# Optimization experiments

Hardware: AMD Instinct MI355X
Metric: run time of the kernel (lower is better)

Reference implementation:

```python
import jax, jax.numpy as jnp
import numpy as np

D_MODEL = 1536
BLOCK = 3
N_BLOCKS = D_MODEL // BLOCK
BATCH = 8192
EPS = 1e-8


def setup_inputs() -> dict:
    key = jax.random.key(0)
    ks = jax.random.split(key, 6)
    s = 1.0 / np.sqrt(D_MODEL)  # torch Linear default-ish scale
    x = jax.random.normal(ks[0], (BATCH, D_MODEL), dtype=jnp.float32)
    h_prev = jax.random.normal(ks[1], (BATCH, D_MODEL), dtype=jnp.float32)
    W_biv = jax.random.normal(ks[2], (D_MODEL, D_MODEL), dtype=jnp.float32) * s
    b_biv = jnp.zeros((D_MODEL,), dtype=jnp.float32)  # init.zeros_
    W_dec = jax.random.normal(ks[3], (1, D_MODEL), dtype=jnp.float32) * s
    b_dec = jnp.full((1,), 1.4, dtype=jnp.float32)  # init.constant_(1.4)
    W_in = jax.random.normal(ks[4], (D_MODEL, D_MODEL), dtype=jnp.float32) * s
    b_in = jax.random.normal(ks[5], (D_MODEL,), dtype=jnp.float32) * s
    return {"x": x, "h_prev": h_prev, "W_biv": W_biv, "b_biv": b_biv,
            "W_dec": W_dec, "b_dec": b_dec, "W_in": W_in, "b_in": b_in}


def _quat_rotate_blocks(h_blocks, bivectors):
    # h_blocks, bivectors: (batch, n_blocks, 3)
    norm_b = jnp.maximum(jnp.linalg.norm(bivectors, axis=-1, keepdims=True), EPS)
    half_angle = norm_b / 2
    w = jnp.cos(half_angle)[..., 0]
    s = (jnp.sin(half_angle) / norm_b)[..., 0]  # sin_ha_over_norm[..., 0]
    # NOTE: faithful to source — qx/qy/qz all use component 0 of sin_ha_over_norm
    qx = s * bivectors[..., 2]
    qy = -s * bivectors[..., 1]
    qz = s * bivectors[..., 0]
    vx, vy, vz = h_blocks[..., 0], h_blocks[..., 1], h_blocks[..., 2]
    tx = 2 * (qy * vz - qz * vy)
    ty = 2 * (qz * vx - qx * vz)
    tz = 2 * (qx * vy - qy * vx)
    rx = vx + w * tx + (qy * tz - qz * ty)
    ry = vy + w * ty + (qz * tx - qx * tz)
    rz = vz + w * tz + (qx * ty - qy * tx)
    return jnp.stack([rx, ry, rz], axis=-1)


def reference(x, h_prev, W_biv, b_biv, W_dec, b_dec, W_in, b_in):
    batch = x.shape[0]
    bivectors = (x @ W_biv.T + b_biv).reshape(batch, N_BLOCKS, 3)
    decay = jax.nn.sigmoid(x @ W_dec.T + b_dec)          # (batch, 1)
    injection = x @ W_in.T + b_in                        # (batch, d_model)
    h_blocks = h_prev.reshape(batch, N_BLOCKS, 3)
    rotated = _quat_rotate_blocks(h_blocks, bivectors)
    return decay * rotated.reshape(batch, D_MODEL) + injection
```

## Files before the change

### kernel.cpp

```cpp
#include <hip/hip_runtime.h>
#include <cstdint>

#define D_MODEL 1536
#define BATCH   8192
#define EPS     1e-8f

#define BM 128
#define BN 96
#define BK 64
#define NT (D_MODEL / BK)
#define NTN (D_MODEL / BN)
#define NTM (BATCH / BM)
#define BUF 40960

typedef __attribute__((ext_vector_type(8))) short bf16x8;
typedef __attribute__((ext_vector_type(8))) unsigned short ushort8;
typedef __attribute__((ext_vector_type(4))) float f32x4;

__device__ __forceinline__ unsigned short f2bf(float f) {
  unsigned u = __builtin_bit_cast(unsigned, f);
  u += 0x7fffu + ((u >> 16) & 1u);
  return (unsigned short)(u >> 16);
}

__device__ __forceinline__ ushort8 pack8u(float4 a, float4 b) {
  ushort8 o;
  o[0] = f2bf(a.x); o[1] = f2bf(a.y); o[2] = f2bf(a.z); o[3] = f2bf(a.w);
  o[4] = f2bf(b.x); o[5] = f2bf(b.y); o[6] = f2bf(b.z); o[7] = f2bf(b.w);
  return o;
}

__device__ __forceinline__ void full_drain() {
  asm volatile("s_waitcnt vmcnt(0) lgkmcnt(0)" ::: "memory");
}
__device__ __forceinline__ void vm_drain() {
  asm volatile("s_waitcnt vmcnt(0)" ::: "memory");
}
__device__ __forceinline__ void lgkm_drain() {
  asm volatile("s_waitcnt lgkmcnt(0)" ::: "memory");
}

__device__ __forceinline__ void load_lds16(const void* g, void* l) {
  __builtin_amdgcn_global_load_lds(
      (const __attribute__((address_space(1))) unsigned int*)g,
      (__attribute__((address_space(3))) unsigned int*)l,
      16, 0, 0);
}

__global__ void prep_all(const float* __restrict__ x,
                         const float* __restrict__ wdec,
                         const float* __restrict__ bdec,
                         const float* __restrict__ wbiv,
                         const float* __restrict__ win,
                         unsigned short* __restrict__ xb,
                         unsigned short* __restrict__ wb,
                         float* __restrict__ decay) {
  const int b = blockIdx.x;
  if (b < 2048) {
    int row  = (int)((b * 256 + threadIdx.x) >> 6);
    int lane = threadIdx.x & 63;
    const float4* xr = (const float4*)(x + (long)row * D_MODEL);
    const float4* wr = (const float4*)wdec;
    unsigned short* xo = xb + (long)row * D_MODEL;
    float acc = 0.f;
#pragma unroll
    for (int i = 0; i < 6; ++i) {
      float4 a = xr[lane + 64 * i];
      float4 w = wr[lane + 64 * i];
      acc += a.x * w.x + a.y * w.y + a.z * w.z + a.w * w.w;
      ushort4 o;
      o.x = f2bf(a.x); o.y = f2bf(a.y); o.z = f2bf(a.z); o.w = f2bf(a.w);
      *(ushort4*)(xo + (lane + 64 * i) * 4) = o;
    }
    for (int off = 32; off; off >>= 1) acc += __shfl_xor(acc, off);
    if (lane == 0) decay[row] = 1.f / (1.f + expf(-(acc + bdec[0])));
  } else {
    const long NW4 = (long)D_MODEL * D_MODEL / 4;
    for (long i = (long)(b - 2048) * 256 + threadIdx.x; i < 2 * NW4;
         i += (long)1024 * 256) {
      const float4* src = (i < NW4) ? (const float4*)wbiv : (const float4*)win;
      long j = (i < NW4) ? i : (i - NW4);
      float4 v = src[j];
      ushort4 o;
      o.x = f2bf(v.x); o.y = f2bf(v.y); o.z = f2bf(v.z); o.w = f2bf(v.w);
      *(ushort4*)(wb + 4 * i) = o;
    }
  }
}

__global__ __launch_bounds__(512, 2)
void fused_main(const unsigned short* __restrict__ xb,
                const unsigned short* __restrict__ wb,
                const float* __restrict__ hprev,
                const float* __restrict__ decay,
                const float* __restrict__ bbiv,
                const float* __restrict__ bin,
                float* __restrict__ out) {
  __shared__ __align__(16) char smem[2 * BUF];
  float* sBv = (float*)smem;

  const int bid = blockIdx.x;
  const int tm = bid / NTN, tn = bid % NTN;
  const int m0 = tm * BM, n0 = tn * BN;
  const int tid  = threadIdx.x;
  const int lane = tid & 63, wid = tid >> 6;
  const int wr = wid >> 1, wc = wid & 1;
  const int lr = lane & 15;
  const int lk = lane >> 4;

  const unsigned short* gptr[5];
  int doff[5];
#pragma unroll
  for (int i = 0; i < 5; ++i) {
    int f = i * 512 + tid;
    if (f < 1024) {
      int row = f >> 3, c = f & 7, cs = c ^ (row & 7);
      gptr[i] = xb + (long)(m0 + row) * D_MODEL + cs * 8;
      doff[i] = f << 4;
    } else if (f < 1792) {
      int g = f - 1024;
      int row = g >> 3, c = g & 7, cs = c ^ (row & 7);
      gptr[i] = wb + (long)(n0 + row) * D_MODEL + cs * 8;
      doff[i] = 16384 + (g << 4);
    } else {
      int g = f - 1792;
      int row = g >> 3, c = g & 7, cs = c ^ (row & 7);
      gptr[i] = wb + (long)D_MODEL * D_MODEL + (long)(n0 + row) * D_MODEL + cs * 8;
      doff[i] = 28672 + (g << 4);
    }
  }

  auto STAGE = [&](int bb) {
#pragma unroll
    for (int i = 0; i < 5; ++i) {
      load_lds16(gptr[i], smem + bb + doff[i]);
      gptr[i] += BK;
    }
  };

  int offA[2][2], offB1[3][2], offB2[3][2];
#pragma unroll
  for (int ks = 0; ks < 2; ++ks) {
    const int slot = ks * 4 + lk;
#pragma unroll
    for (int mi = 0; mi < 2; ++mi) {
      int R = wr * 32 + mi * 16 + lr;
      offA[mi][ks] = (R * 64 + (slot ^ (R & 7)) * 8) * 2;
    }
#pragma unroll
    for (int ni = 0; ni < 3; ++ni) {
      int R = wc * 48 + ni * 16 + lr;
      int o = (R * 64 + (slot ^ (R & 7)) * 8) * 2;
      offB1[ni][ks] = 16384 + o;
      offB2[ni][ks] = 28672 + o;
    }
  }

  f32x4 accB[2][3], accI[2][3];
#pragma unroll
  for (int a = 0; a < 2; ++a)
#pragma unroll
    for (int b = 0; b < 3; ++b) { accB[a][b] = (f32x4)0.f; accI[a][b] = (f32x4)0.f; }

  STAGE(0);
  vm_drain();
  __syncthreads();

  for (int t = 0; t < NT; ++t) {
    const int cur = (t & 1) * BUF;
    if (t + 1 < NT) STAGE(((t + 1) & 1) * BUF);

#pragma unroll
    for (int ks = 0; ks < 2; ++ks) {
      bf16x8 a[2], b1[3], b2[3];
#pragma unroll
      for (int mi = 0; mi < 2; ++mi)
        a[mi] = *(const bf16x8*)(smem + cur + offA[mi][ks]);
#pragma unroll
      for (int ni = 0; ni < 3; ++ni) {
        b1[ni] = *(const bf16x8*)(smem + cur + offB1[ni][ks]);
        b2[ni] = *(const bf16x8*)(smem + cur + offB2[ni][ks]);
      }
      lgkm_drain();
      __builtin_amdgcn_sched_barrier(0);
#pragma unroll
      for (int mi = 0; mi < 2; ++mi)
#pragma unroll
        for (int ni = 0; ni < 3; ++ni)
          accB[mi][ni] = __builtin_amdgcn_mfma_f32_16x16x32_bf16(
              a[mi], b1[ni], accB[mi][ni], 0, 0, 0);
      __builtin_amdgcn_sched_barrier(0);
#pragma unroll
      for (int mi = 0; mi < 2; ++mi)
#pragma unroll
        for (int ni = 0; ni < 3; ++ni)
          accI[mi][ni] = __builtin_amdgcn_mfma_f32_16x16x32_bf16(
              a[mi], b2[ni], accI[mi][ni], 0, 0, 0);
      __builtin_amdgcn_sched_barrier(0);
    }

    vm_drain();
    __syncthreads();
  }

#pragma unroll
  for (int mi = 0; mi < 2; ++mi)
#pragma unroll
    for (int ni = 0; ni < 3; ++ni) {
      int col = wc * 48 + ni * 16 + lr;
      float bb = bbiv[n0 + col];
#pragma unroll
      for (int r = 0; r < 4; ++r) {
        int row = wr * 32 + mi * 16 + lk * 4 + r;
        sBv[row * 97 + col] = accB[mi][ni][r] + bb;
      }
    }
  full_drain();
  __syncthreads();

#pragma unroll
  for (int mi = 0; mi < 2; ++mi)
#pragma unroll
    for (int ni = 0; ni < 3; ++ni) {
      int col  = wc * 48 + ni * 16 + lr;
      int gcol = n0 + col;
      int c    = (col % 3);
      int lc0  = col - c;
      float binv = bin[gcol];
#pragma unroll
      for (int r = 0; r < 4; ++r) {
        int row  = wr * 32 + mi * 16 + lk * 4 + r;
        int grow = m0 + row;
        float bx = sBv[row * 97 + lc0];
        float by = sBv[row * 97 + lc0 + 1];
        float bz = sBv[row * 97 + lc0 + 2];
        const float* hp = hprev + (long)grow * D_MODEL + (n0 + lc0);
        float vx = hp[0], vy = hp[1], vz = hp[2];
        float nb = sqrtf(bx * bx + by * by + bz * bz);
        nb = fmaxf(nb, EPS);
        float ha = 0.5f * nb;
        float w  = __cosf(ha);
        float s  = __sinf(ha) / nb;
        float qx = s * bz, qy = -s * by, qz = s * bx;
        float tx = 2.f * (qy * vz - qz * vy);
        float ty = 2.f * (qz * vx - qx * vz);
        float tz = 2.f * (qx * vy - qy * vx);
        float rx = vx + w * tx + (qy * tz - qz * ty);
        float ry = vy + w * ty + (qz * tx - qx * tz);
        float rz = vz + w * tz + (qx * ty - qy * tx);
        float rc = (c == 0) ? rx : ((c == 1) ? ry : rz);
        out[(long)grow * D_MODEL + gcol] =
            decay[grow] * rc + (accI[mi][ni][r] + binv);
      }
    }
}

__global__ __launch_bounds__(256, 2)
void fused_mfma3(const float* __restrict__ x,
                 const float* __restrict__ wbiv,
                 const float* __restrict__ win,
                 const float* __restrict__ hprev,
                 const float* __restrict__ wdec,
                 const float* __restrict__ bdec,
                 const float* __restrict__ bbiv,
                 const float* __restrict__ bin,
                 float* __restrict__ out) {
  __shared__ __align__(16) char smem[50688];
  __shared__ float sDecay[BM];
  unsigned short* sA  = (unsigned short*)smem;
  unsigned short* sB1 = (unsigned short*)(smem + 16384);
  unsigned short* sB2 = (unsigned short*)(smem + 28672);
  float* sBv = (float*)smem;

  const int bid = blockIdx.x;
  const int tm = bid / NTN, tn = bid % NTN;
  const int m0 = tm * BM, n0 = tn * BN;
  const int tid  = threadIdx.x;
  const int lane = tid & 63, wid = tid >> 6;
  const int wr = wid >> 1, wc = wid & 1;
  const int lr = lane & 15;
  const int lk = lane >> 4;

  {
    const float bd = bdec[0];
    const float4* wd4 = (const float4*)wdec;
    for (int rr = 0; rr < 32; ++rr) {
      int row = wid * 32 + rr;
      const float4* xr = (const float4*)(x + (long)(m0 + row) * D_MODEL);
      float acc = 0.f;
#pragma unroll
      for (int i = 0; i < 6; ++i) {
        float4 a = xr[lane + 64 * i];
        float4 b = wd4[lane + 64 * i];
        acc += a.x * b.x + a.y * b.y + a.z * b.z + a.w * b.w;
      }
      for (int off = 32; off; off >>= 1) acc += __shfl_xor(acc, off);
      if (lane == 0) sDecay[row] = 1.f / (1.f + expf(-(acc + bd)));
    }
  }

  f32x4 accB[4][3], accI[4][3];
#pragma unroll
  for (int a = 0; a < 4; ++a)
#pragma unroll
    for (int b = 0; b < 3; ++b) { accB[a][b] = (f32x4)0.f; accI[a][b] = (f32x4)0.f; }

  for (int kt = 0; kt < D_MODEL; kt += 64) {
    full_drain();
    __syncthreads();
#pragma unroll
    for (int i = 0; i < 4; ++i) {
      int f = i * 256 + tid;
      int row = f >> 3, c = f & 7;
      const float4* p = (const float4*)(x + (long)(m0 + row) * D_MODEL + kt + c * 8);
      *(ushort8*)(sA + row * 64 + c * 8) = pack8u(p[0], p[1]);
    }
#pragma unroll
    for (int i = 0; i < 6; ++i) {
      int mat = (i >= 3);
      int g = (i - 3 * mat) * 256 + tid;
      int row = g >> 3, c = g & 7;
      const float* wsrc = mat ? win : wbiv;
      const float4* p = (const float4*)(wsrc + (long)(n0 + row) * D_MODEL + kt + c * 8);
      *(ushort8*)((mat ? sB2 : sB1) + row * 64 + c * 8) = pack8u(p[0], p[1]);
    }
    full_drain();
    __syncthreads();

#pragma unroll
    for (int ks = 0; ks < 2; ++ks) {
      const int k0 = ks * 32 + lk * 8;
      bf16x8 a[4], b1[3], b2[3];
#pragma unroll
      for (int mi = 0; mi < 4; ++mi)
        a[mi] = *(const bf16x8*)(sA + (wr * 64 + mi * 16 + lr) * 64 + k0);
#pragma unroll
      for (int ni = 0; ni < 3; ++ni) {
        b1[ni] = *(const bf16x8*)(sB1 + (wc * 48 + ni * 16 + lr) * 64 + k0);
        b2[ni] = *(const bf16x8*)(sB2 + (wc * 48 + ni * 16 + lr) * 64 + k0);
      }
      full_drain();
      __builtin_amdgcn_sched_barrier(0);
#pragma unroll
      for (int mi = 0; mi < 4; ++mi)
#pragma unroll
        for (int ni = 0; ni < 3; ++ni)
          accB[mi][ni] = __builtin_amdgcn_mfma_f32_16x16x32_bf16(
              a[mi], b1[ni], accB[mi][ni], 0, 0, 0);
      __builtin_amdgcn_sched_barrier(0);
#pragma unroll
      for (int mi = 0; mi < 4; ++mi)
#pragma unroll
        for (int ni = 0; ni < 3; ++ni)
          accI[mi][ni] = __builtin_amdgcn_mfma_f32_16x16x32_bf16(
              a[mi], b2[ni], accI[mi][ni], 0, 0, 0);
      __builtin_amdgcn_sched_barrier(0);
    }
  }

  full_drain();
  __syncthreads();
#pragma unroll
  for (int mi = 0; mi < 4; ++mi)
#pragma unroll
    for (int ni = 0; ni < 3; ++ni) {
      int col = wc * 48 + ni * 16 + lr;
      float bb = bbiv[n0 + col];
#pragma unroll
      for (int r = 0; r < 4; ++r) {
        int row = wr * 64 + mi * 16 + lk * 4 + r;
        sBv[row * 97 + col] = accB[mi][ni][r] + bb;
      }
    }
  full_drain();
  __syncthreads();

#pragma unroll
  for (int mi = 0; mi < 4; ++mi)
#pragma unroll
    for (int ni = 0; ni < 3; ++ni) {
      int col  = wc * 48 + ni * 16 + lr;
      int gcol = n0 + col;
      int c    = (col % 3);
      int lc0  = col - c;
      float binv = bin[gcol];
#pragma unroll
      for (int r = 0; r < 4; ++r) {
        int row  = wr * 64 + mi * 16 + lk * 4 + r;
        int grow = m0 + row;
        float bx = sBv[row * 97 + lc0];
        float by = sBv[row * 97 + lc0 + 1];
        float bz = sBv[row * 97 + lc0 + 2];
        const float* hp = hprev + (long)grow * D_MODEL + (n0 + lc0);
        float vx = hp[0], vy = hp[1], vz = hp[2];
        float nb = sqrtf(bx * bx + by * by + bz * bz);
        nb = fmaxf(nb, EPS);
        float ha = 0.5f * nb;
        float w  = cosf(ha);
        float s  = sinf(ha) / nb;
        float qx = s * bz, qy = -s * by, qz = s * bx;
        float tx = 2.f * (qy * vz - qz * vy);
        float ty = 2.f * (qz * vx - qx * vz);
        float tz = 2.f * (qx * vy - qy * vx);
        float rx = vx + w * tx + (qy * tz - qz * ty);
        float ry = vy + w * ty + (qz * tx - qx * tz);
        float rz = vz + w * tz + (qx * ty - qy * tx);
        float rc = (c == 0) ? rx : ((c == 1) ? ry : rz);
        out[(long)grow * D_MODEL + gcol] =
            sDecay[row] * rc + (accI[mi][ni][r] + binv);
      }
    }
}

extern "C" void kernel_launch(void* const* d_in, const int* in_sizes, int n_in,
                              void* d_out, int out_size, void* d_ws, size_t ws_size,
                              hipStream_t stream) {
  const float* x     = (const float*)d_in[0];
  const float* hprev = (const float*)d_in[1];
  const float* wbiv  = (const float*)d_in[2];
  const float* bbiv  = (const float*)d_in[3];
  const float* wdec  = (const float*)d_in[4];
  const float* bdec  = (const float*)d_in[5];
  const float* win   = (const float*)d_in[6];
  const float* bin   = (const float*)d_in[7];
  float* out = (float*)d_out;

  const size_t XB_B  = 25165824;
  const size_t WB_B  = 9437184;
  const size_t DC_B  = 32768;

  if (ws_size >= XB_B + WB_B + DC_B) {
    char* ws = (char*)d_ws;
    unsigned short* xb = (unsigned short*)ws;
    unsigned short* wb = (unsigned short*)(ws + XB_B);
    float* decay       = (float*)(ws + XB_B + WB_B);
    prep_all<<<dim3(3072), dim3(256), 0, stream>>>(
        x, wdec, bdec, wbiv, win, xb, wb, decay);
    fused_main<<<dim3(NTM * NTN), dim3(512), 0, stream>>>(
        xb, wb, hprev, decay, bbiv, bin, out);
  } else {
    fused_mfma3<<<dim3(NTM * NTN), dim3(256), 0, stream>>>(
        x, wbiv, win, hprev, wdec, bdec, bbiv, bin, out);
  }
}
```

Measured before the change: 113.5 us.

## Double M tile to 256 rows with 1024-thread blocks for weight reuse

Raises the fused GEMM block tile from 128 to 256 batch rows and uses 16 waves per block, so each staged tile of the two weight matrices is shared by twice as many rows. The aim is to cut global and LDS traffic for weights per output element. In exchange, occupancy drops to one block per CU, the LDS footprint grows to about 112 KB, and the grid halves, which may worsen latency hiding and tail balance.

Measured after the change: 113.2 us (median of 2 runs). No clear change (-0.3%).

```diff
diff --git a/kernel.cpp b/kernel.cpp
--- a/kernel.cpp
+++ b/kernel.cpp
@@ -5,13 +5,15 @@
 #define BATCH   8192
 #define EPS     1e-8f
 
+#define BMM 256
+#define BN  96
+#define BK  64
+#define NT  (D_MODEL / BK)
+#define NTN (D_MODEL / BN)
+#define NTMM (BATCH / BMM)
+#define BUF 57344
 #define BM 128
-#define BN 96
-#define BK 64
-#define NT (D_MODEL / BK)
-#define NTN (D_MODEL / BN)
 #define NTM (BATCH / BM)
-#define BUF 40960
 
 typedef __attribute__((ext_vector_type(8))) short bf16x8;
 typedef __attribute__((ext_vector_type(8))) unsigned short ushort8;
@@ -88,7 +90,7 @@
   }
 }
 
-__global__ __launch_bounds__(512, 2)
+__global__ __launch_bounds__(1024, 1)
 void fused_main(const unsigned short* __restrict__ xb,
                 const unsigned short* __restrict__ wb,
                 const float* __restrict__ hprev,
@@ -96,46 +98,53 @@
                 const float* __restrict__ bbiv,
                 const float* __restrict__ bin,
                 float* __restrict__ out) {
-  __shared__ __align__(16) char smem[2 * BUF];
+  __shared__ __align__(16) char smem[114688];
   float* sBv = (float*)smem;
 
   const int bid = blockIdx.x;
   const int tm = bid / NTN, tn = bid % NTN;
-  const int m0 = tm * BM, n0 = tn * BN;
+  const int m0 = tm * BMM, n0 = tn * BN;
   const int tid  = threadIdx.x;
   const int lane = tid & 63, wid = tid >> 6;
   const int wr = wid >> 1, wc = wid & 1;
   const int lr = lane & 15;
   const int lk = lane >> 4;
 
-  const unsigned short* gptr[5];
-  int doff[5];
-#pragma unroll
-  for (int i = 0; i < 5; ++i) {
-    int f = i * 512 + tid;
-    if (f < 1024) {
+  const unsigned short* gptr[4];
+  int doff[4];
+  {
+#pragma unroll
+    for (int i = 0; i < 2; ++i) {
+      int f = i * 1024 + tid;
       int row = f >> 3, c = f & 7, cs = c ^ (row & 7);
       gptr[i] = xb + (long)(m0 + row) * D_MODEL + cs * 8;
       doff[i] = f << 4;
-    } else if (f < 1792) {
-      int g = f - 1024;
+    }
+    if (tid < 768) {
+      int g = tid;
       int row = g >> 3, c = g & 7, cs = c ^ (row & 7);
-      gptr[i] = wb + (long)(n0 + row) * D_MODEL + cs * 8;
-      doff[i] = 16384 + (g << 4);
+      gptr[2] = wb + (long)(n0 + row) * D_MODEL + cs * 8;
+      doff[2] = 32768 + (g << 4);
     } else {
-      int g = f - 1792;
+      int g = tid - 768;
       int row = g >> 3, c = g & 7, cs = c ^ (row & 7);
-      gptr[i] = wb + (long)D_MODEL * D_MODEL + (long)(n0 + row) * D_MODEL + cs * 8;
-      doff[i] = 28672 + (g << 4);
+      gptr[2] = wb + (long)D_MODEL * D_MODEL + (long)(n0 + row) * D_MODEL + cs * 8;
+      doff[2] = 45056 + (g << 4);
+    }
+    {
+      int g = 256 + tid;
+      int row = g >> 3, c = g & 7, cs = c ^ (row & 7);
+      gptr[3] = wb + (long)D_MODEL * D_MODEL + (long)(n0 + row) * D_MODEL + cs * 8;
+      doff[3] = 45056 + (g << 4);
     }
   }
 
   auto STAGE = [&](int bb) {
-#pragma unroll
-    for (int i = 0; i < 5; ++i) {
-      load_lds16(gptr[i], smem + bb + doff[i]);
-      gptr[i] += BK;
-    }
+    load_lds16(gptr[0], smem + bb + doff[0]);
+    load_lds16(gptr[1], smem + bb + doff[1]);
+    load_lds16(gptr[2], smem + bb + doff[2]);
+    if (tid < 512) load_lds16(gptr[3], smem + bb + doff[3]);
+    gptr[0] += BK; gptr[1] += BK; gptr[2] += BK; gptr[3] += BK;
   };
 
   int offA[2][2], offB1[3][2], offB2[3][2];
@@ -151,8 +160,8 @@
     for (int ni = 0; ni < 3; ++ni) {
       int R = wc * 48 + ni * 16 + lr;
       int o = (R * 64 + (slot ^ (R & 7)) * 8) * 2;
-      offB1[ni][ks] = 16384 + o;
-      offB2[ni][ks] = 28672 + o;
+      offB1[ni][ks] = 32768 + o;
+      offB2[ni][ks] = 45056 + o;
     }
   }
 
@@ -436,7 +445,7 @@
     float* decay       = (float*)(ws + XB_B + WB_B);
     prep_all<<<dim3(3072), dim3(256), 0, stream>>>(
         x, wdec, bdec, wbiv, win, xb, wb, decay);
-    fused_main<<<dim3(NTM * NTN), dim3(512), 0, stream>>>(
+    fused_main<<<dim3(NTMM * NTN), dim3(1024), 0, stream>>>(
         xb, wb, hprev, decay, bbiv, bin, out);
   } else {
     fused_mfma3<<<dim3(NTM * NTN), dim3(256), 0, stream>>>(
```
